# Kernel optimization log

Hardware: AMD Instinct MI355X
Metric: run time of the kernel (lower is better)

## Reference

```python
import jax, jax.numpy as jnp
import numpy as np


def _pick(key, nodes, mask, cnt):
    # Uniformly pick one of the `cnt` entries of `nodes` where mask is True.
    r = jax.random.randint(key, (), 0, jnp.maximum(cnt, 1))
    cs = jnp.cumsum(mask.astype(jnp.int32))
    return nodes[jnp.argmax(cs == r + 1)]


def _one_walk(key, nbrs, f0, n_faces, L):
    # nbrs: [N,3] int32 neighbor table, f0: scalar start face.
    seq = jnp.zeros((L + 1,), jnp.int32).at[0].set(f0)
    visited = jnp.zeros((n_faces + 1,), bool).at[n_faces].set(True).at[f0].set(True)

    def cond(st):
        return st[2] <= L

    def body(st):
        seq, visited, i, bs, k = st
        k, k1, k2, k3 = jax.random.split(k, 4)
        cur = seq[i - 1]
        nb = nbrs[cur]                     # [3] neighbor candidates
        unv = ~visited[nb]
        cnt = unv.sum()
        need = cnt == 0                    # stuck -> backtrack
        cand = _pick(k1, nb, unv, cnt)

        def bcond(c):
            bs_c, found = c[0], c[1]
            return need & (~found) & (i > bs_c)

        def bbody(c):
            bs_c, found, ta, kk = c
            kk, kp = jax.random.split(kk)
            back = seq[i - bs_c - 1]
            bn = nbrs[back]
            bm = ~visited[bn]
            bc = bm.sum()
            f2 = bc > 0
            ta2 = _pick(kp, bn, bm, bc)
            return (jnp.where(f2, bs_c, bs_c + 2), f2, jnp.where(f2, ta2, ta), kk)

        bs_f, found, ta_bt, _ = jax.lax.while_loop(
            bcond, bbody, (bs, jnp.array(False), jnp.int32(0), k2))
        rand_node = jax.random.randint(k3, (), 0, n_faces, dtype=jnp.int32)
        to_add = jnp.where(~need, cand, jnp.where(found, ta_bt, rand_node))
        hit = need & found                 # successful backtrack
        bs_new = jnp.where(hit, bs_f, jnp.int32(1))
        i_new = jnp.where(hit, i - bs_f, i)
        ar = jnp.arange(L + 1, dtype=jnp.int32)
        # torch: replace seq[i-bs:i] with to_add on successful backtrack
        seq = jnp.where(hit & (ar >= i_new) & (ar < i), to_add, seq)
        visited = visited.at[to_add].set(True)
        seq = seq.at[i_new].set(to_add)
        return (seq, visited, i_new + 1, bs_new, k)

    seq, *_ = jax.lax.while_loop(
        cond, body, (seq, visited, jnp.int32(1), jnp.int32(1), key))
    return seq


def patch_random_walk(key, neighbors, centers, n_faces, seq_len):
    B, G = centers.shape
    keys = jax.random.split(key, B * G).reshape(B, G)
    walk_g = jax.vmap(_one_walk, in_axes=(0, None, 0, None, None))
    walk_bg = jax.vmap(walk_g, in_axes=(0, 0, 0, None, None))
    return walk_bg(keys, neighbors, centers, n_faces, seq_len)  # [B,G,L+1] int32


def setup_inputs() -> dict:
    key = jax.random.key(0)
    k1, k2, k3 = jax.random.split(key, 3)
    B, N, G = 4, 20000, 1024
    xyz = jax.random.normal(k1, (B, N, 3), dtype=jnp.float32)
    neighbors = jax.random.randint(k2, (B, N, 3), 0, N, dtype=jnp.int32)
    centers = jax.random.randint(k3, (B, G), 0, N, dtype=jnp.int32)
    return {"xyz": xyz, "neighbors": neighbors, "centers": centers,
            "n_faces": N, "seq_len": 63}


def reference(xyz, neighbors, centers, n_faces, seq_len):
    # patch_random_walk -> idx [B,G,K]; then Group.forward gather + recenter.
    idx = patch_random_walk(jax.random.key(42), neighbors, centers, n_faces, seq_len)
    gather = jax.vmap(lambda p, i: p[i])(xyz, idx)            # [B,G,K,3]
    center_xyz = jax.vmap(lambda p, c: p[c])(xyz, centers)    # [B,G,3]
    return gather - center_xyz[:, :, None, :]
```

## Files before the change

### kernel.cpp

```cpp
#include <hip/hip_runtime.h>
#include <stdint.h>
#include <stddef.h>


namespace {

__device__ __forceinline__ uint32_t rotl32(uint32_t x, int r) {
  return (x << r) | (x >> (32 - r));
}

__device__ __forceinline__ void tf2x32(uint32_t ka, uint32_t kb,
                                       uint32_t x0, uint32_t x1,
                                       uint32_t& o0, uint32_t& o1) {
  const uint32_t kc = ka ^ kb ^ 0x1BD11BDAu;
  x0 += ka; x1 += kb;
#define TF_R4(r0, r1, r2, r3)                          \
  x0 += x1; x1 = rotl32(x1, r0); x1 ^= x0;             \
  x0 += x1; x1 = rotl32(x1, r1); x1 ^= x0;             \
  x0 += x1; x1 = rotl32(x1, r2); x1 ^= x0;             \
  x0 += x1; x1 = rotl32(x1, r3); x1 ^= x0;
  TF_R4(13, 15, 26, 6)  x0 += kb; x1 += kc + 1u;
  TF_R4(17, 29, 16, 24) x0 += kc; x1 += ka + 2u;
  TF_R4(13, 15, 26, 6)  x0 += ka; x1 += kb + 3u;
  TF_R4(17, 29, 16, 24) x0 += kb; x1 += kc + 4u;
  TF_R4(13, 15, 26, 6)  x0 += kc; x1 += ka + 5u;
#undef TF_R4
  o0 = x0; o1 = x1;
}

__device__ __forceinline__ void randbits(uint32_t ka, uint32_t kb,
                                         uint32_t& hi, uint32_t& lo) {
  uint32_t s0a, s0b, s1a, s1b, h0, h1;
  tf2x32(ka, kb, 0u, 0u, s0a, s0b);
  tf2x32(ka, kb, 0u, 1u, s1a, s1b);
  tf2x32(s0a, s0b, 0u, 0u, h0, h1);
  hi = h0 ^ h1;
  tf2x32(s1a, s1b, 0u, 0u, h0, h1);
  lo = h0 ^ h1;
}

__device__ __forceinline__ uint32_t r_generic(uint32_t hi, uint32_t lo,
                                              uint32_t span) {
  uint32_t mult = 65536u % span;
  mult = (mult * mult) % span;
  return ((hi % span) * mult + (lo % span)) % span;
}

__device__ __forceinline__ uint32_t pick_code(uint32_t hi, uint32_t lo) {
  return ((hi % 3u + lo % 3u) % 3u) | ((lo & 1u) << 2);
}

constexpr int WPB = 16;
constexpr int CH = 64;
constexpr int NMAX = 20352;
constexpr int VISW = 636;

__global__ __launch_bounds__(1024) void walk_kernel(
    const float* __restrict__ xyz, const int* __restrict__ nbrs,
    const int* __restrict__ centers, const int* __restrict__ n_faces_p,
    const int* __restrict__ seq_len_p, float* __restrict__ out,
    int s0, int num_walks, int Lp1) {
  __shared__ uint32_t nb01L[NMAX];
  __shared__ uint16_t nb2L[NMAX];
  __shared__ uint32_t visL[WPB * VISW];

  const int tid = threadIdx.x;
  const int wv = tid >> 6, lane = tid & 63;
  const int w0 = blockIdx.x * WPB;
  if (w0 >= num_walks) return;
  const int w = w0 + wv;
  const bool active = (w < num_walks);

  const int N = *n_faces_p;
  const int L = *seq_len_p;
  const int B = s0 / (3 * N);
  const int G = num_walks / B;
  const bool lds_ok = (N <= NMAX) && (G % WPB == 0);

  const int bb = (active ? w : w0) / G;
  const int* __restrict__ nb   = nbrs + (size_t)bb * N * 3;
  const float* __restrict__ xb = xyz + (size_t)bb * N * 3;

  const int f0 = active ? centers[w] : 0;
  int3 grow = make_int3(0, 0, 0);
  if (!lds_ok && active)
    grow = *reinterpret_cast<const int3*>(nb + 3 * (size_t)f0);

  if (wv == 0) {
    if (lane < WPB && (w0 + lane) < num_walks) {
      uint32_t ka, kb;
      tf2x32(0u, 42u, 0u, (uint32_t)(w0 + lane), ka, kb);
      visL[(lane * CH + 0) * 2 + 0] = ka;
      visL[(lane * CH + 0) * 2 + 1] = kb;
#pragma clang loop unroll(disable)
      for (int c2 = 1; c2 < CH; ++c2) {
        tf2x32(ka, kb, 0u, 0u, ka, kb);
        visL[(lane * CH + c2) * 2 + 0] = ka;
        visL[(lane * CH + c2) * 2 + 1] = kb;
      }
    }
  } else if (lds_ok) {
    for (int r = tid - 64; r < N; r += 960) {
      const int3 v = *reinterpret_cast<const int3*>(nb + 3 * (size_t)r);
      nb01L[r] = (uint32_t)v.x | ((uint32_t)v.y << 16);
      nb2L[r]  = (uint16_t)v.z;
    }
  }
  __syncthreads();

  const uint32_t mka = visL[(wv * CH + lane) * 2 + 0];
  const uint32_t mkb = visL[(wv * CH + lane) * 2 + 1];
  uint32_t mycode;
  {
    uint32_t k1a, k1b, hi, lo;
    tf2x32(mka, mkb, 0u, 1u, k1a, k1b);
    randbits(k1a, k1b, hi, lo);
    mycode = pick_code(hi, lo);
  }
  __syncthreads();

  if (!active) return;

  uint32_t extka = 0, extkb = 0;
  int extc = -1;
  auto get_key = [&](int idx, uint32_t& ra, uint32_t& rb) {
    if (idx < CH) {
      ra = (uint32_t)__shfl((int)mka, idx);
      rb = (uint32_t)__shfl((int)mkb, idx);
    } else {
      if (extc < 0) {
        extka = (uint32_t)__shfl((int)mka, CH - 1);
        extkb = (uint32_t)__shfl((int)mkb, CH - 1);
        extc = CH - 1;
      }
      while (extc < idx) { tf2x32(extka, extkb, 0u, 0u, extka, extkb); ++extc; }
      ra = extka; rb = extkb;
    }
  };

  int seqr = (lane == 0) ? f0 : -1;
  uint32_t code_next = (uint32_t)__shfl((int)mycode, 0);
  int i = 1, bs = 1, c = 0;

  if (lds_ok) {
    uint32_t* __restrict__ visW = visL + wv * VISW;
    for (int j = lane; j < VISW; j += 64) visW[j] = 0u;
    if (lane == 0) visW[(unsigned)f0 >> 5] = 1u << (f0 & 31);

    uint32_t p0 = nb01L[f0];
    int n0 = (int)(p0 & 0xffffu), n1 = (int)(p0 >> 16), n2 = (int)nb2L[f0];

    while (i <= L) {
      const int idx = c; ++c;
      const uint32_t pA = nb01L[n0]; const uint32_t a2 = nb2L[n0];
      const uint32_t pB = nb01L[n1]; const uint32_t b2 = nb2L[n1];
      const uint32_t pC = nb01L[n2]; const uint32_t c2v = nb2L[n2];
      const uint32_t wv0 = visW[(unsigned)n0 >> 5];
      const uint32_t wv1 = visW[(unsigned)n1 >> 5];
      const uint32_t wv2 = visW[(unsigned)n2 >> 5];
      const uint32_t codeP = code_next;
      code_next = (uint32_t)__shfl((int)mycode, (c < CH) ? c : 0);

      const uint32_t u0 = ((wv0 >> (n0 & 31)) & 1u) ^ 1u;
      const uint32_t u1 = ((wv1 >> (n1 & 31)) & 1u) ^ 1u;
      const uint32_t u2 = ((wv2 >> (n2 & 31)) & 1u) ^ 1u;
      const uint32_t cnt = u0 + u1 + u2;

      int to_add, sel;
      if (__builtin_expect(cnt == 0, 0)) {
        sel = -1;
        uint32_t kia, kib;
        get_key(idx, kia, kib);
        uint32_t kka, kkb;
        tf2x32(kia, kib, 0u, 2u, kka, kkb);
        bool found = false;
        int ta = 0, bsc = bs;
        while (!found && i > bsc) {
          uint32_t ca, cb, kpa, kpb;
          tf2x32(kka, kkb, 0u, 0u, ca, cb);
          tf2x32(kka, kkb, 0u, 1u, kpa, kpb);
          const int back = __shfl(seqr, i - bsc - 1);
          const uint32_t pm = nb01L[back];
          const int m0 = (int)(pm & 0xffffu), m1 = (int)(pm >> 16);
          const int m2 = (int)nb2L[back];
          const uint32_t e0 = ((visW[(unsigned)m0 >> 5] >> (m0 & 31)) & 1u) ^ 1u;
          const uint32_t e1 = ((visW[(unsigned)m1 >> 5] >> (m1 & 31)) & 1u) ^ 1u;
          const uint32_t e2 = ((visW[(unsigned)m2 >> 5] >> (m2 & 31)) & 1u) ^ 1u;
          const uint32_t bc = e0 + e1 + e2;
          if (bc > 0) {
            uint32_t bhi, blo;
            randbits(kpa, kpb, bhi, blo);
            const uint32_t bcode = pick_code(bhi, blo);
            const uint32_t r3 = bcode & 3u, r2 = (bcode >> 2) & 1u;
            const uint32_t t2v = (bc == 3 ? r3 : (bc == 2 ? r2 : 0)) + 1;
            ta = (e0 == t2v) ? m0 : ((e0 + e1 == t2v) ? m1 : m2);
            found = true;
          } else {
            bsc += 2;
          }
          kka = ca; kkb = cb;
        }
        if (found) {
          to_add = ta;
          const int i_new = i - bsc;
          seqr = (lane >= i_new && lane < i) ? to_add : seqr;
          bs = bsc; i = i_new;
        } else {
          uint32_t k3a, k3b, rhi, rlo;
          tf2x32(kia, kib, 0u, 3u, k3a, k3b);
          randbits(k3a, k3b, rhi, rlo);
          to_add = (int)r_generic(rhi, rlo, (uint32_t)N);
          bs = 1;
        }
        if (lane == 0)
          visW[(unsigned)to_add >> 5] |= 1u << (to_add & 31);
        seqr = (lane == i) ? to_add : seqr;
        ++i;
        const uint32_t p = nb01L[to_add];
        n0 = (int)(p & 0xffffu); n1 = (int)(p >> 16); n2 = (int)nb2L[to_add];
        continue;
      }
      uint32_t code = codeP;
      if (__builtin_expect(idx >= CH, 0)) {
        uint32_t ia, ib, k1a, k1b, hi, lo;
        get_key(idx, ia, ib);
        tf2x32(ia, ib, 0u, 1u, k1a, k1b);
        randbits(k1a, k1b, hi, lo);
        code = pick_code(hi, lo);
      }
      const uint32_t r3 = code & 3u, r2 = (code >> 2) & 1u;
      const uint32_t target = (cnt == 3 ? r3 : (cnt == 2 ? r2 : 0)) + 1;
      sel = (u0 == target) ? 0 : ((u0 + u1 == target) ? 1 : 2);
      to_add = (sel == 0) ? n0 : ((sel == 1) ? n1 : n2);
      const uint32_t wsel = (sel == 0) ? wv0 : ((sel == 1) ? wv1 : wv2);
      if (lane == 0)
        visW[(unsigned)to_add >> 5] = wsel | (1u << (to_add & 31));
      seqr = (lane == i) ? to_add : seqr;
      bs = 1; ++i;
      if (sel == 0)      { n0 = (int)(pA & 0xffffu); n1 = (int)(pA >> 16); n2 = (int)a2; }
      else if (sel == 1) { n0 = (int)(pB & 0xffffu); n1 = (int)(pB >> 16); n2 = (int)b2; }
      else               { n0 = (int)(pC & 0xffffu); n1 = (int)(pC >> 16); n2 = (int)c2v; }
    }
  } else {
    int hist  = (lane == 0) ? f0 : -1;
    int hist2 = -1;
    int3 row = grow;
    while (i <= L) {
      const int idx = c; ++c;
      const bool deep = (idx >= CH);
      const uint32_t codeP = code_next;
      code_next = (uint32_t)__shfl((int)mycode, (c < CH) ? c : 0);

      const int n0 = row.x, n1 = row.y, n2 = row.z;
      int v0 = __any(hist == n0), v1 = __any(hist == n1), v2 = __any(hist == n2);
      if (deep) {
        v0 |= __any(hist2 == n0); v1 |= __any(hist2 == n1); v2 |= __any(hist2 == n2);
      }
      const int u0 = 1 - v0, u1 = 1 - v1, u2 = 1 - v2;
      const int cnt = u0 + u1 + u2;

      int to_add;
      bool hit = false;
      int bsf = bs;
      if (cnt > 0) {
        uint32_t code = codeP;
        if (deep) {
          uint32_t ia, ib, k1a, k1b, hi, lo;
          get_key(idx, ia, ib);
          tf2x32(ia, ib, 0u, 1u, k1a, k1b);
          randbits(k1a, k1b, hi, lo);
          code = pick_code(hi, lo);
        }
        const int r3 = (int)(code & 3u), r2 = (int)((code >> 2) & 1u);
        const int target = (cnt == 3 ? r3 : (cnt == 2 ? r2 : 0)) + 1;
        to_add = (u0 == target) ? n0 : ((u0 + u1 == target) ? n1 : n2);
      } else {
        uint32_t kia, kib;
        get_key(idx, kia, kib);
        uint32_t kka, kkb;
        tf2x32(kia, kib, 0u, 2u, kka, kkb);
        bool found = false;
        int ta = 0, bsc = bs;
        while (!found && i > bsc) {
          uint32_t ca, cb, kpa, kpb;
          tf2x32(kka, kkb, 0u, 0u, ca, cb);
          tf2x32(kka, kkb, 0u, 1u, kpa, kpb);
          const int back = __shfl(seqr, i - bsc - 1);
          const int3 br = *reinterpret_cast<const int3*>(nb + 3 * (size_t)back);
          int w0m = __any(hist == br.x), w1m = __any(hist == br.y), w2m = __any(hist == br.z);
          if (deep) {
            w0m |= __any(hist2 == br.x); w1m |= __any(hist2 == br.y); w2m |= __any(hist2 == br.z);
          }
          const int e0 = 1 - w0m, e1 = 1 - w1m, e2 = 1 - w2m;
          const int bc = e0 + e1 + e2;
          if (bc > 0) {
            uint32_t bhi, blo;
            randbits(kpa, kpb, bhi, blo);
            const uint32_t bcode = pick_code(bhi, blo);
            const int r3 = (int)(bcode & 3u), r2 = (int)((bcode >> 2) & 1u);
            const int t2v = (bc == 3 ? r3 : (bc == 2 ? r2 : 0)) + 1;
            ta = (e0 == t2v) ? br.x : ((e0 + e1 == t2v) ? br.y : br.z);
            found = true;
          } else {
            bsc += 2;
          }
          kka = ca; kkb = cb;
        }
        if (found) {
          to_add = ta; hit = true; bsf = bsc;
        } else {
          uint32_t k3a, k3b, rhi, rlo;
          tf2x32(kia, kib, 0u, 3u, k3a, k3b);
          randbits(k3a, k3b, rhi, rlo);
          to_add = (int)r_generic(rhi, rlo, (uint32_t)N);
        }
      }

      int i_new, up;
      if (hit) { i_new = i - bsf; bs = bsf; up = i - 1; }
      else     { i_new = i;       bs = 1;   up = i; }
      seqr = (lane >= i_new && lane <= up) ? to_add : seqr;

      const int slot = idx + 1;
      if (slot < CH)          hist  = (lane == slot)      ? to_add : hist;
      else if (slot < 2 * CH) hist2 = (lane == slot - CH) ? to_add : hist2;

      i = i_new + 1;
      row = *reinterpret_cast<const int3*>(nb + 3 * (size_t)to_add);
    }
  }

  const float cx = xb[3 * (size_t)f0 + 0];
  const float cy = xb[3 * (size_t)f0 + 1];
  const float cz = xb[3 * (size_t)f0 + 2];
  if (lane < Lp1) {
    const int node = seqr;
    float3 v;
    v.x = xb[3 * (size_t)node + 0] - cx;
    v.y = xb[3 * (size_t)node + 1] - cy;
    v.z = xb[3 * (size_t)node + 2] - cz;
    *reinterpret_cast<float3*>(out + ((size_t)w * Lp1 + lane) * 3) = v;
  }
}

}

extern "C" void kernel_launch(void* const* d_in, const int* in_sizes, int n_in,
                              void* d_out, int out_size, void* d_ws, size_t ws_size,
                              hipStream_t stream) {
  const float* xyz     = (const float*)d_in[0];
  const int*   nbrs    = (const int*)d_in[1];
  const int*   centers = (const int*)d_in[2];
  const int*   n_faces = (const int*)d_in[3];
  const int*   seq_len = (const int*)d_in[4];
  float* out = (float*)d_out;

  const int s0 = in_sizes[0];
  const int num_walks = in_sizes[2];
  const int Lp1 = out_size / (3 * num_walks);

  const int blocks = (num_walks + WPB - 1) / WPB;
  walk_kernel<<<blocks, WPB * 64, 0, stream>>>(
      xyz, nbrs, centers, n_faces, seq_len, out, s0, num_walks, Lp1);
}
```

Measured before the change: 99.40 us.

## Run 16 walks per wavefront lane-parallel with 256-thread blocks and streamed outputs

Blocks shrink from 1024 to 256 threads, and the 16 walks of a block now run one per lane inside a single wavefront instead of one walk per wavefront. Per-step pick codes are precomputed into LDS and packed into registers, the walk sequence is kept in LDS, and output coordinates are written as each step is taken rather than gathered at the end. The intent is to cut the cost of staging the neighbour table (fewer idle waves per block, more blocks resident) and to drop the cross-lane shuffles. The trade-off is that walks in one wavefront now diverge, stalling on whichever walker backtracks longest, and NMAX is tightened to exactly 20000.

```diff
diff --git a/kernel.cpp b/kernel.cpp
--- a/kernel.cpp
+++ b/kernel.cpp
@@ -52,10 +52,11 @@
 
 constexpr int WPB = 16;
 constexpr int CH = 64;
-constexpr int NMAX = 20352;
-constexpr int VISW = 636;
-
-__global__ __launch_bounds__(1024) void walk_kernel(
+constexpr int NMAX = 20000;
+constexpr int VISW = 625;
+constexpr int THREADS = 256;
+
+__global__ __launch_bounds__(256) void walk_kernel(
     const float* __restrict__ xyz, const int* __restrict__ nbrs,
     const int* __restrict__ centers, const int* __restrict__ n_faces_p,
     const int* __restrict__ seq_len_p, float* __restrict__ out,
@@ -63,28 +64,19 @@
   __shared__ uint32_t nb01L[NMAX];
   __shared__ uint16_t nb2L[NMAX];
   __shared__ uint32_t visL[WPB * VISW];
+  __shared__ uint16_t seqL[WPB][CH + 4];
 
   const int tid = threadIdx.x;
   const int wv = tid >> 6, lane = tid & 63;
   const int w0 = blockIdx.x * WPB;
   if (w0 >= num_walks) return;
-  const int w = w0 + wv;
-  const bool active = (w < num_walks);
 
   const int N = *n_faces_p;
   const int L = *seq_len_p;
   const int B = s0 / (3 * N);
   const int G = num_walks / B;
-  const bool lds_ok = (N <= NMAX) && (G % WPB == 0);
-
-  const int bb = (active ? w : w0) / G;
-  const int* __restrict__ nb   = nbrs + (size_t)bb * N * 3;
-  const float* __restrict__ xb = xyz + (size_t)bb * N * 3;
-
-  const int f0 = active ? centers[w] : 0;
-  int3 grow = make_int3(0, 0, 0);
-  if (!lds_ok && active)
-    grow = *reinterpret_cast<const int3*>(nb + 3 * (size_t)f0);
+  const bool lds_ok = (N <= NMAX) && (G % WPB == 0) && (L < CH);
+  const int bb0 = w0 / G;
 
   if (wv == 0) {
     if (lane < WPB && (w0 + lane) < num_walks) {
@@ -100,246 +92,356 @@
       }
     }
   } else if (lds_ok) {
-    for (int r = tid - 64; r < N; r += 960) {
-      const int3 v = *reinterpret_cast<const int3*>(nb + 3 * (size_t)r);
+    const int* __restrict__ nbT = nbrs + (size_t)bb0 * N * 3;
+    for (int r = tid - 64; r < N; r += (THREADS - 64)) {
+      const int3 v = *reinterpret_cast<const int3*>(nbT + 3 * (size_t)r);
       nb01L[r] = (uint32_t)v.x | ((uint32_t)v.y << 16);
       nb2L[r]  = (uint16_t)v.z;
     }
   }
   __syncthreads();
 
-  const uint32_t mka = visL[(wv * CH + lane) * 2 + 0];
-  const uint32_t mkb = visL[(wv * CH + lane) * 2 + 1];
-  uint32_t mycode;
-  {
-    uint32_t k1a, k1b, hi, lo;
-    tf2x32(mka, mkb, 0u, 1u, k1a, k1b);
-    randbits(k1a, k1b, hi, lo);
-    mycode = pick_code(hi, lo);
-  }
-  __syncthreads();
-
-  if (!active) return;
-
-  uint32_t extka = 0, extkb = 0;
-  int extc = -1;
-  auto get_key = [&](int idx, uint32_t& ra, uint32_t& rb) {
-    if (idx < CH) {
-      ra = (uint32_t)__shfl((int)mka, idx);
-      rb = (uint32_t)__shfl((int)mkb, idx);
-    } else {
-      if (extc < 0) {
-        extka = (uint32_t)__shfl((int)mka, CH - 1);
-        extkb = (uint32_t)__shfl((int)mkb, CH - 1);
-        extc = CH - 1;
-      }
-      while (extc < idx) { tf2x32(extka, extkb, 0u, 0u, extka, extkb); ++extc; }
-      ra = extka; rb = extkb;
-    }
-  };
-
-  int seqr = (lane == 0) ? f0 : -1;
-  uint32_t code_next = (uint32_t)__shfl((int)mycode, 0);
-  int i = 1, bs = 1, c = 0;
-
   if (lds_ok) {
-    uint32_t* __restrict__ visW = visL + wv * VISW;
-    for (int j = lane; j < VISW; j += 64) visW[j] = 0u;
-    if (lane == 0) visW[(unsigned)f0 >> 5] = 1u << (f0 & 31);
-
-    uint32_t p0 = nb01L[f0];
+    uint8_t* const codesB = reinterpret_cast<uint8_t*>(&visL[2048]);
+#pragma unroll
+    for (int p = 0; p < (WPB * CH) / THREADS; ++p) {
+      const int pair = tid + THREADS * p;
+      const int wk = pair >> 6, st = pair & 63;
+      if ((w0 + wk) < num_walks) {
+        const uint32_t ka = visL[(wk * CH + st) * 2 + 0];
+        const uint32_t kb = visL[(wk * CH + st) * 2 + 1];
+        uint32_t k1a, k1b, hi, lo;
+        tf2x32(ka, kb, 0u, 1u, k1a, k1b);
+        randbits(k1a, k1b, hi, lo);
+        codesB[wk * CH + st] = (uint8_t)pick_code(hi, lo);
+      }
+    }
+    __syncthreads();
+
+    const int w = w0 + lane;
+    const bool walker = (wv == 0) && (lane < WPB) && (w < num_walks);
+    uint32_t cw[7] = {0, 0, 0, 0, 0, 0, 0};
+    uint32_t k0a = 0, k0b = 0;
+    if (walker) {
+      tf2x32(0u, 42u, 0u, (uint32_t)w, k0a, k0b);
+      const uint32_t* cwd = &visL[2048 + lane * (CH / 4)];
+#pragma unroll
+      for (int t = 0; t < CH / 4; ++t) {
+        const uint32_t wd = cwd[t];
+#pragma unroll
+        for (int b = 0; b < 4; ++b) {
+          const int s = 4 * t + b;
+          const uint32_t c3 = (wd >> (8 * b)) & 7u;
+          cw[s / 10] |= c3 << (3 * (s % 10));
+        }
+      }
+    }
+    __syncthreads();
+    for (int j = tid; j < WPB * VISW; j += THREADS) visL[j] = 0u;
+    __syncthreads();
+    if (wv != 0) return;
+
+    const float* __restrict__ xb = xyz + (size_t)bb0 * N * 3;
+    const int f0 = walker ? centers[w] : 0;
+    uint32_t* __restrict__ visW = visL + (walker ? lane : 0) * VISW;
+
+    float cx = 0.f, cy = 0.f, cz = 0.f;
+    if (walker) {
+      cx = xb[3 * (size_t)f0 + 0];
+      cy = xb[3 * (size_t)f0 + 1];
+      cz = xb[3 * (size_t)f0 + 2];
+      visW[(unsigned)f0 >> 5] = 1u << (f0 & 31);
+      seqL[lane][0] = (uint16_t)f0;
+      float3 z; z.x = 0.f; z.y = 0.f; z.z = 0.f;
+      *reinterpret_cast<float3*>(out + (size_t)w * Lp1 * 3) = z;
+    }
+
+    const uint32_t p0 = nb01L[f0];
     int n0 = (int)(p0 & 0xffffu), n1 = (int)(p0 >> 16), n2 = (int)nb2L[f0];
-
-    while (i <= L) {
-      const int idx = c; ++c;
-      const uint32_t pA = nb01L[n0]; const uint32_t a2 = nb2L[n0];
-      const uint32_t pB = nb01L[n1]; const uint32_t b2 = nb2L[n1];
-      const uint32_t pC = nb01L[n2]; const uint32_t c2v = nb2L[n2];
-      const uint32_t wv0 = visW[(unsigned)n0 >> 5];
-      const uint32_t wv1 = visW[(unsigned)n1 >> 5];
-      const uint32_t wv2 = visW[(unsigned)n2 >> 5];
-      const uint32_t codeP = code_next;
-      code_next = (uint32_t)__shfl((int)mycode, (c < CH) ? c : 0);
-
-      const uint32_t u0 = ((wv0 >> (n0 & 31)) & 1u) ^ 1u;
-      const uint32_t u1 = ((wv1 >> (n1 & 31)) & 1u) ^ 1u;
-      const uint32_t u2 = ((wv2 >> (n2 & 31)) & 1u) ^ 1u;
+    uint32_t pA01 = nb01L[n0], pB01 = nb01L[n1], pC01 = nb01L[n2];
+    uint32_t pA2 = nb2L[n0], pB2 = nb2L[n1], pC2 = nb2L[n2];
+    uint32_t wd0 = visW[(unsigned)n0 >> 5];
+    uint32_t wd1 = visW[(unsigned)n1 >> 5];
+    uint32_t wd2 = visW[(unsigned)n2 >> 5];
+
+    int i = walker ? 1 : (L + 1);
+    int bs = 1;
+    int extc = 0; uint32_t extka = k0a, extkb = k0b;
+    bool pend = false; float3 pg; uint32_t ppos = 0;
+
+    for (int c = 0;; ++c) {
+      if (!__any(i <= L)) break;
+      const bool act = (i <= L);
+
+      if (pend) {
+        float3 v; v.x = pg.x - cx; v.y = pg.y - cy; v.z = pg.z - cz;
+        *reinterpret_cast<float3*>(out + (size_t)ppos * 3) = v;
+        pend = false;
+      }
+
+      const uint32_t u0 = ((wd0 >> (n0 & 31)) & 1u) ^ 1u;
+      const uint32_t u1 = ((wd1 >> (n1 & 31)) & 1u) ^ 1u;
+      const uint32_t u2 = ((wd2 >> (n2 & 31)) & 1u) ^ 1u;
       const uint32_t cnt = u0 + u1 + u2;
 
-      int to_add, sel;
-      if (__builtin_expect(cnt == 0, 0)) {
-        sel = -1;
-        uint32_t kia, kib;
-        get_key(idx, kia, kib);
-        uint32_t kka, kkb;
-        tf2x32(kia, kib, 0u, 2u, kka, kkb);
-        bool found = false;
-        int ta = 0, bsc = bs;
-        while (!found && i > bsc) {
-          uint32_t ca, cb, kpa, kpb;
-          tf2x32(kka, kkb, 0u, 0u, ca, cb);
-          tf2x32(kka, kkb, 0u, 1u, kpa, kpb);
-          const int back = __shfl(seqr, i - bsc - 1);
-          const uint32_t pm = nb01L[back];
-          const int m0 = (int)(pm & 0xffffu), m1 = (int)(pm >> 16);
-          const int m2 = (int)nb2L[back];
-          const uint32_t e0 = ((visW[(unsigned)m0 >> 5] >> (m0 & 31)) & 1u) ^ 1u;
-          const uint32_t e1 = ((visW[(unsigned)m1 >> 5] >> (m1 & 31)) & 1u) ^ 1u;
-          const uint32_t e2 = ((visW[(unsigned)m2 >> 5] >> (m2 & 31)) & 1u) ^ 1u;
-          const uint32_t bc = e0 + e1 + e2;
-          if (bc > 0) {
-            uint32_t bhi, blo;
-            randbits(kpa, kpb, bhi, blo);
-            const uint32_t bcode = pick_code(bhi, blo);
-            const uint32_t r3 = bcode & 3u, r2 = (bcode >> 2) & 1u;
-            const uint32_t t2v = (bc == 3 ? r3 : (bc == 2 ? r2 : 0)) + 1;
-            ta = (e0 == t2v) ? m0 : ((e0 + e1 == t2v) ? m1 : m2);
-            found = true;
-          } else {
-            bsc += 2;
-          }
-          kka = ca; kkb = cb;
-        }
-        if (found) {
-          to_add = ta;
-          const int i_new = i - bsc;
-          seqr = (lane >= i_new && lane < i) ? to_add : seqr;
-          bs = bsc; i = i_new;
-        } else {
+      uint32_t code;
+      if (__builtin_expect(c < CH, 1)) {
+        const int wi = c / 10;
+        const int sh = 3 * (c - wi * 10);
+        uint32_t cwv = cw[0];
+        cwv = (wi == 1) ? cw[1] : cwv;  cwv = (wi == 2) ? cw[2] : cwv;
+        cwv = (wi == 3) ? cw[3] : cwv;  cwv = (wi == 4) ? cw[4] : cwv;
+        cwv = (wi == 5) ? cw[5] : cwv;  cwv = (wi == 6) ? cw[6] : cwv;
+        code = (cwv >> sh) & 7u;
+      } else {
+        while (extc < c) { tf2x32(extka, extkb, 0u, 0u, extka, extkb); ++extc; }
+        uint32_t k1a, k1b, hi, lo;
+        tf2x32(extka, extkb, 0u, 1u, k1a, k1b);
+        randbits(k1a, k1b, hi, lo);
+        code = pick_code(hi, lo);
+      }
+
+      const bool need = act && (cnt == 0u);
+      if (__builtin_expect(__any(need), 0)) {
+        while (extc < c) { tf2x32(extka, extkb, 0u, 0u, extka, extkb); ++extc; }
+        const uint32_t kia = extka, kib = extkb;
+        bool found = false; int ta = 0; int bsc = bs;
+        if (need) {
+          uint32_t kka, kkb;
+          tf2x32(kia, kib, 0u, 2u, kka, kkb);
+          while (!found && i > bsc) {
+            uint32_t ca, cb, kpa, kpb;
+            tf2x32(kka, kkb, 0u, 0u, ca, cb);
+            tf2x32(kka, kkb, 0u, 1u, kpa, kpb);
+            const int back = (int)seqL[lane][i - bsc - 1];
+            const uint32_t pm = nb01L[back];
+            const int m0 = (int)(pm & 0xffffu), m1 = (int)(pm >> 16);
+            const int m2 = (int)nb2L[back];
+            const uint32_t e0 = ((visW[(unsigned)m0 >> 5] >> (m0 & 31)) & 1u) ^ 1u;
+            const uint32_t e1 = ((visW[(unsigned)m1 >> 5] >> (m1 & 31)) & 1u) ^ 1u;
+            const uint32_t e2 = ((visW[(unsigned)m2 >> 5] >> (m2 & 31)) & 1u) ^ 1u;
+            const uint32_t bc = e0 + e1 + e2;
+            if (bc > 0) {
+              uint32_t bhi, blo;
+              randbits(kpa, kpb, bhi, blo);
+              const uint32_t bcode = pick_code(bhi, blo);
+              const uint32_t br3 = bcode & 3u, br2 = (bcode >> 2) & 1u;
+              const uint32_t t2v = (bc == 3 ? br3 : (bc == 2 ? br2 : 0)) + 1;
+              ta = (e0 == t2v) ? m0 : ((e0 + e1 == t2v) ? m1 : m2);
+              found = true;
+            } else {
+              bsc += 2;
+            }
+            kka = ca; kkb = cb;
+          }
+        }
+        int rnd = 0;
+        if (need && !found) {
           uint32_t k3a, k3b, rhi, rlo;
           tf2x32(kia, kib, 0u, 3u, k3a, k3b);
           randbits(k3a, k3b, rhi, rlo);
-          to_add = (int)r_generic(rhi, rlo, (uint32_t)N);
-          bs = 1;
-        }
-        if (lane == 0)
-          visW[(unsigned)to_add >> 5] |= 1u << (to_add & 31);
-        seqr = (lane == i) ? to_add : seqr;
-        ++i;
-        const uint32_t p = nb01L[to_add];
-        n0 = (int)(p & 0xffffu); n1 = (int)(p >> 16); n2 = (int)nb2L[to_add];
-        continue;
-      }
-      uint32_t code = codeP;
-      if (__builtin_expect(idx >= CH, 0)) {
-        uint32_t ia, ib, k1a, k1b, hi, lo;
-        get_key(idx, ia, ib);
-        tf2x32(ia, ib, 0u, 1u, k1a, k1b);
+          rnd = (int)r_generic(rhi, rlo, (uint32_t)N);
+        }
+        const uint32_t r3 = code & 3u, r2 = (code >> 2) & 1u;
+        const uint32_t tgt = (cnt == 3 ? r3 : (cnt == 2 ? r2 : 0)) + 1;
+        const int selc = (u0 == tgt) ? 0 : ((u0 + u1 == tgt) ? 1 : 2);
+        const int to_add_c = (selc == 0) ? n0 : ((selc == 1) ? n1 : n2);
+        const uint32_t wselc = (selc == 0) ? wd0 : ((selc == 1) ? wd1 : wd2);
+
+        const bool hit = need && found;
+        const int to_add = need ? (found ? ta : rnd) : to_add_c;
+
+        if (act) {
+          uint32_t wdf = need ? visW[(unsigned)to_add >> 5] : wselc;
+          visW[(unsigned)to_add >> 5] = wdf | (1u << (to_add & 31));
+          if (hit) {
+            const int i_new = i - bsc;
+            const float3 p = *reinterpret_cast<const float3*>(
+                xb + 3 * (size_t)to_add);
+            float3 v; v.x = p.x - cx; v.y = p.y - cy; v.z = p.z - cz;
+            for (int j = i_new; j < i; ++j) {
+              seqL[lane][j] = (uint16_t)to_add;
+              *reinterpret_cast<float3*>(
+                  out + ((size_t)w * Lp1 + j) * 3) = v;
+            }
+            bs = bsc; i = i_new + 1;
+          } else {
+            seqL[lane][i] = (uint16_t)to_add;
+            pg = *reinterpret_cast<const float3*>(xb + 3 * (size_t)to_add);
+            pend = true; ppos = (uint32_t)(w * Lp1 + i);
+            bs = 1; ++i;
+          }
+        }
+        const int rn = act ? to_add : 0;
+        const uint32_t pr = nb01L[rn];
+        const uint32_t pr2 = nb2L[rn];
+        if (act) {
+          n0 = (int)(pr & 0xffffu); n1 = (int)(pr >> 16); n2 = (int)pr2;
+        }
+      } else {
+        const uint32_t r3 = code & 3u, r2 = (code >> 2) & 1u;
+        const uint32_t tgt = (cnt == 3 ? r3 : (cnt == 2 ? r2 : 0)) + 1;
+        const int sel = (u0 == tgt) ? 0 : ((u0 + u1 == tgt) ? 1 : 2);
+        const int to_add = (sel == 0) ? n0 : ((sel == 1) ? n1 : n2);
+        const uint32_t wsel = (sel == 0) ? wd0 : ((sel == 1) ? wd1 : wd2);
+        if (act) {
+          visW[(unsigned)to_add >> 5] = wsel | (1u << (to_add & 31));
+          seqL[lane][i] = (uint16_t)to_add;
+          pg = *reinterpret_cast<const float3*>(xb + 3 * (size_t)to_add);
+          pend = true; ppos = (uint32_t)(w * Lp1 + i);
+          bs = 1; ++i;
+          if (sel == 0)      { n0 = (int)(pA01 & 0xffffu); n1 = (int)(pA01 >> 16); n2 = (int)pA2; }
+          else if (sel == 1) { n0 = (int)(pB01 & 0xffffu); n1 = (int)(pB01 >> 16); n2 = (int)pB2; }
+          else               { n0 = (int)(pC01 & 0xffffu); n1 = (int)(pC01 >> 16); n2 = (int)pC2; }
+        }
+      }
+      pA01 = nb01L[n0]; pA2 = nb2L[n0];
+      pB01 = nb01L[n1]; pB2 = nb2L[n1];
+      pC01 = nb01L[n2]; pC2 = nb2L[n2];
+      wd0 = visW[(unsigned)n0 >> 5];
+      wd1 = visW[(unsigned)n1 >> 5];
+      wd2 = visW[(unsigned)n2 >> 5];
+    }
+    if (pend) {
+      float3 v; v.x = pg.x - cx; v.y = pg.y - cy; v.z = pg.z - cz;
+      *reinterpret_cast<float3*>(out + (size_t)ppos * 3) = v;
+    }
+  } else {
+    for (int sub = 0; sub < 4; ++sub) {
+      const int w = w0 + 4 * wv + sub;
+      if (w >= num_walks) continue;
+      const int bb = w / G;
+      const int* __restrict__ nbG = nbrs + (size_t)bb * N * 3;
+      const float* __restrict__ xb = xyz + (size_t)bb * N * 3;
+      const int f0 = centers[w];
+      const uint32_t mka = visL[((4 * wv + sub) * CH + lane) * 2 + 0];
+      const uint32_t mkb = visL[((4 * wv + sub) * CH + lane) * 2 + 1];
+      uint32_t mycode;
+      {
+        uint32_t k1a, k1b, hi, lo;
+        tf2x32(mka, mkb, 0u, 1u, k1a, k1b);
         randbits(k1a, k1b, hi, lo);
-        code = pick_code(hi, lo);
-      }
-      const uint32_t r3 = code & 3u, r2 = (code >> 2) & 1u;
-      const uint32_t target = (cnt == 3 ? r3 : (cnt == 2 ? r2 : 0)) + 1;
-      sel = (u0 == target) ? 0 : ((u0 + u1 == target) ? 1 : 2);
-      to_add = (sel == 0) ? n0 : ((sel == 1) ? n1 : n2);
-      const uint32_t wsel = (sel == 0) ? wv0 : ((sel == 1) ? wv1 : wv2);
-      if (lane == 0)
-        visW[(unsigned)to_add >> 5] = wsel | (1u << (to_add & 31));
-      seqr = (lane == i) ? to_add : seqr;
-      bs = 1; ++i;
-      if (sel == 0)      { n0 = (int)(pA & 0xffffu); n1 = (int)(pA >> 16); n2 = (int)a2; }
-      else if (sel == 1) { n0 = (int)(pB & 0xffffu); n1 = (int)(pB >> 16); n2 = (int)b2; }
-      else               { n0 = (int)(pC & 0xffffu); n1 = (int)(pC >> 16); n2 = (int)c2v; }
-    }
-  } else {
-    int hist  = (lane == 0) ? f0 : -1;
-    int hist2 = -1;
-    int3 row = grow;
-    while (i <= L) {
-      const int idx = c; ++c;
-      const bool deep = (idx >= CH);
-      const uint32_t codeP = code_next;
-      code_next = (uint32_t)__shfl((int)mycode, (c < CH) ? c : 0);
-
-      const int n0 = row.x, n1 = row.y, n2 = row.z;
-      int v0 = __any(hist == n0), v1 = __any(hist == n1), v2 = __any(hist == n2);
-      if (deep) {
-        v0 |= __any(hist2 == n0); v1 |= __any(hist2 == n1); v2 |= __any(hist2 == n2);
-      }
-      const int u0 = 1 - v0, u1 = 1 - v1, u2 = 1 - v2;
-      const int cnt = u0 + u1 + u2;
-
-      int to_add;
-      bool hit = false;
-      int bsf = bs;
-      if (cnt > 0) {
-        uint32_t code = codeP;
+        mycode = pick_code(hi, lo);
+      }
+      uint32_t extka = 0, extkb = 0;
+      int extc = -1;
+      auto get_key = [&](int idxk, uint32_t& ra, uint32_t& rb) {
+        if (idxk < CH) {
+          ra = (uint32_t)__shfl((int)mka, idxk);
+          rb = (uint32_t)__shfl((int)mkb, idxk);
+        } else {
+          if (extc < 0) {
+            extka = (uint32_t)__shfl((int)mka, CH - 1);
+            extkb = (uint32_t)__shfl((int)mkb, CH - 1);
+            extc = CH - 1;
+          }
+          while (extc < idxk) { tf2x32(extka, extkb, 0u, 0u, extka, extkb); ++extc; }
+          ra = extka; rb = extkb;
+        }
+      };
+
+      int seqr = (lane == 0) ? f0 : -1;
+      uint32_t code_next = (uint32_t)__shfl((int)mycode, 0);
+      int i = 1, bs = 1, c = 0;
+      int hist  = (lane == 0) ? f0 : -1;
+      int hist2 = -1;
+      int3 row = *reinterpret_cast<const int3*>(nbG + 3 * (size_t)f0);
+      while (i <= L) {
+        const int idx = c; ++c;
+        const bool deep = (idx >= CH);
+        const uint32_t codeP = code_next;
+        code_next = (uint32_t)__shfl((int)mycode, (c < CH) ? c : 0);
+
+        const int n0 = row.x, n1 = row.y, n2 = row.z;
+        int v0 = __any(hist == n0), v1 = __any(hist == n1), v2 = __any(hist == n2);
         if (deep) {
-          uint32_t ia, ib, k1a, k1b, hi, lo;
-          get_key(idx, ia, ib);
-          tf2x32(ia, ib, 0u, 1u, k1a, k1b);
-          randbits(k1a, k1b, hi, lo);
-          code = pick_code(hi, lo);
-        }
-        const int r3 = (int)(code & 3u), r2 = (int)((code >> 2) & 1u);
-        const int target = (cnt == 3 ? r3 : (cnt == 2 ? r2 : 0)) + 1;
-        to_add = (u0 == target) ? n0 : ((u0 + u1 == target) ? n1 : n2);
-      } else {
-        uint32_t kia, kib;
-        get_key(idx, kia, kib);
-        uint32_t kka, kkb;
-        tf2x32(kia, kib, 0u, 2u, kka, kkb);
-        bool found = false;
-        int ta = 0, bsc = bs;
-        while (!found && i > bsc) {
-          uint32_t ca, cb, kpa, kpb;
-          tf2x32(kka, kkb, 0u, 0u, ca, cb);
-          tf2x32(kka, kkb, 0u, 1u, kpa, kpb);
-          const int back = __shfl(seqr, i - bsc - 1);
-          const int3 br = *reinterpret_cast<const int3*>(nb + 3 * (size_t)back);
-          int w0m = __any(hist == br.x), w1m = __any(hist == br.y), w2m = __any(hist == br.z);
+          v0 |= __any(hist2 == n0); v1 |= __any(hist2 == n1); v2 |= __any(hist2 == n2);
+        }
+        const int u0 = 1 - v0, u1 = 1 - v1, u2 = 1 - v2;
+        const int cnt = u0 + u1 + u2;
+
+        int to_add;
+        bool hit = false;
+        int bsf = bs;
+        if (cnt > 0) {
+          uint32_t code = codeP;
           if (deep) {
-            w0m |= __any(hist2 == br.x); w1m |= __any(hist2 == br.y); w2m |= __any(hist2 == br.z);
-          }
-          const int e0 = 1 - w0m, e1 = 1 - w1m, e2 = 1 - w2m;
-          const int bc = e0 + e1 + e2;
-          if (bc > 0) {
-            uint32_t bhi, blo;
-            randbits(kpa, kpb, bhi, blo);
-            const uint32_t bcode = pick_code(bhi, blo);
-            const int r3 = (int)(bcode & 3u), r2 = (int)((bcode >> 2) & 1u);
-            const int t2v = (bc == 3 ? r3 : (bc == 2 ? r2 : 0)) + 1;
-            ta = (e0 == t2v) ? br.x : ((e0 + e1 == t2v) ? br.y : br.z);
-            found = true;
+            uint32_t ia, ib, k1a, k1b, hi, lo;
+            get_key(idx, ia, ib);
+            tf2x32(ia, ib, 0u, 1u, k1a, k1b);
+            randbits(k1a, k1b, hi, lo);
+            code = pick_code(hi, lo);
+          }
+          const int r3 = (int)(code & 3u), r2 = (int)((code >> 2) & 1u);
+          const int target = (cnt == 3 ? r3 : (cnt == 2 ? r2 : 0)) + 1;
+          to_add = (u0 == target) ? n0 : ((u0 + u1 == target) ? n1 : n2);
+        } else {
+          uint32_t kia, kib;
+          get_key(idx, kia, kib);
+          uint32_t kka, kkb;
+          tf2x32(kia, kib, 0u, 2u, kka, kkb);
+          bool found = false;
+          int ta = 0, bsc = bs;
+          while (!found && i > bsc) {
+            uint32_t ca, cb, kpa, kpb;
+            tf2x32(kka, kkb, 0u, 0u, ca, cb);
+            tf2x32(kka, kkb, 0u, 1u, kpa, kpb);
+            const int back = __shfl(seqr, i - bsc - 1);
+            const int3 br = *reinterpret_cast<const int3*>(nbG + 3 * (size_t)back);
+            int w0m = __any(hist == br.x), w1m = __any(hist == br.y), w2m = __any(hist == br.z);
+            if (deep) {
+              w0m |= __any(hist2 == br.x); w1m |= __any(hist2 == br.y); w2m |= __any(hist2 == br.z);
+            }
+            const int e0 = 1 - w0m, e1 = 1 - w1m, e2 = 1 - w2m;
+            const int bc = e0 + e1 + e2;
+            if (bc > 0) {
+              uint32_t bhi, blo;
+              randbits(kpa, kpb, bhi, blo);
+              const uint32_t bcode = pick_code(bhi, blo);
+              const int r3 = (int)(bcode & 3u), r2 = (int)((bcode >> 2) & 1u);
+              const int t2v = (bc == 3 ? r3 : (bc == 2 ? r2 : 0)) + 1;
+              ta = (e0 == t2v) ? br.x : ((e0 + e1 == t2v) ? br.y : br.z);
+              found = true;
+            } else {
+              bsc += 2;
+            }
+            kka = ca; kkb = cb;
+          }
+          if (found) {
+            to_add = ta; hit = true; bsf = bsc;
           } else {
-            bsc += 2;
-          }
-          kka = ca; kkb = cb;
-        }
-        if (found) {
-          to_add = ta; hit = true; bsf = bsc;
-        } else {
-          uint32_t k3a, k3b, rhi, rlo;
-          tf2x32(kia, kib, 0u, 3u, k3a, k3b);
-          randbits(k3a, k3b, rhi, rlo);
-          to_add = (int)r_generic(rhi, rlo, (uint32_t)N);
-        }
-      }
-
-      int i_new, up;
-      if (hit) { i_new = i - bsf; bs = bsf; up = i - 1; }
-      else     { i_new = i;       bs = 1;   up = i; }
-      seqr = (lane >= i_new && lane <= up) ? to_add : seqr;
-
-      const int slot = idx + 1;
-      if (slot < CH)          hist  = (lane == slot)      ? to_add : hist;
-      else if (slot < 2 * CH) hist2 = (lane == slot - CH) ? to_add : hist2;
-
-      i = i_new + 1;
-      row = *reinterpret_cast<const int3*>(nb + 3 * (size_t)to_add);
-    }
-  }
-
-  const float cx = xb[3 * (size_t)f0 + 0];
-  const float cy = xb[3 * (size_t)f0 + 1];
-  const float cz = xb[3 * (size_t)f0 + 2];
-  if (lane < Lp1) {
-    const int node = seqr;
-    float3 v;
-    v.x = xb[3 * (size_t)node + 0] - cx;
-    v.y = xb[3 * (size_t)node + 1] - cy;
-    v.z = xb[3 * (size_t)node + 2] - cz;
-    *reinterpret_cast<float3*>(out + ((size_t)w * Lp1 + lane) * 3) = v;
+            uint32_t k3a, k3b, rhi, rlo;
+            tf2x32(kia, kib, 0u, 3u, k3a, k3b);
+            randbits(k3a, k3b, rhi, rlo);
+            to_add = (int)r_generic(rhi, rlo, (uint32_t)N);
+          }
+        }
+
+        int i_new, up;
+        if (hit) { i_new = i - bsf; bs = bsf; up = i - 1; }
+        else     { i_new = i;       bs = 1;   up = i; }
+        seqr = (lane >= i_new && lane <= up) ? to_add : seqr;
+
+        const int slot = idx + 1;
+        if (slot < CH)          hist  = (lane == slot)      ? to_add : hist;
+        else if (slot < 2 * CH) hist2 = (lane == slot - CH) ? to_add : hist2;
+
+        i = i_new + 1;
+        row = *reinterpret_cast<const int3*>(nbG + 3 * (size_t)to_add);
+      }
+
+      const float cx = xb[3 * (size_t)f0 + 0];
+      const float cy = xb[3 * (size_t)f0 + 1];
+      const float cz = xb[3 * (size_t)f0 + 2];
+      if (lane < Lp1) {
+        const int node = seqr;
+        float3 v;
+        v.x = xb[3 * (size_t)node + 0] - cx;
+        v.y = xb[3 * (size_t)node + 1] - cy;
+        v.z = xb[3 * (size_t)node + 2] - cz;
+        *reinterpret_cast<float3*>(out + ((size_t)w * Lp1 + lane) * 3) = v;
+      }
+    }
   }
 }
 
@@ -360,6 +462,6 @@
   const int Lp1 = out_size / (3 * num_walks);
 
   const int blocks = (num_walks + WPB - 1) / WPB;
-  walk_kernel<<<blocks, WPB * 64, 0, stream>>>(
+  walk_kernel<<<blocks, THREADS, 0, stream>>>(
       xyz, nbrs, centers, n_faces, seq_len, out, s0, num_walks, Lp1);
 }
```

After: 111.0 us. +11.7%, slower.
